# Kernel optimization log

Hardware: AMD Instinct MI355X
Metric: run time of the kernel (lower is better)

Reference implementation:

```python
import jax, jax.numpy as jnp
import numpy as np

N = 100000
E = 1600000
D_IN = 128
HEADS = 8
HEAD_DIM = 16  # hidden_channels // heads = 128 // 8
D_HID = HEADS * HEAD_DIM  # 128
D_OUT = 128
NEG_SLOPE = 0.2


def setup_inputs() -> dict:
    key = jax.random.key(0)
    ks = jax.random.split(key, 10)
    x = jax.random.normal(ks[0], (N, D_IN), dtype=jnp.float32)
    edge_index = jax.random.randint(ks[1], (2, E), 0, N, dtype=jnp.int64)
    s = 1.0 / np.sqrt(D_IN)
    W_gat = jax.random.uniform(ks[2], (D_IN, D_HID), minval=-s, maxval=s, dtype=jnp.float32)
    att_src = jax.random.uniform(ks[3], (HEADS, HEAD_DIM), minval=-s, maxval=s, dtype=jnp.float32)
    att_dst = jax.random.uniform(ks[4], (HEADS, HEAD_DIM), minval=-s, maxval=s, dtype=jnp.float32)
    b_gat = jnp.zeros((D_HID,), dtype=jnp.float32)
    so = 1.0 / np.sqrt(D_OUT)
    W_fc1 = jax.random.uniform(ks[5], (D_OUT, D_OUT), minval=-so, maxval=so, dtype=jnp.float32)
    b_fc1 = jax.random.uniform(ks[6], (D_OUT,), minval=-so, maxval=so, dtype=jnp.float32)
    W_fc2 = jax.random.uniform(ks[7], (D_OUT, D_OUT), minval=-so, maxval=so, dtype=jnp.float32)
    b_fc2 = jax.random.uniform(ks[8], (D_OUT,), minval=-so, maxval=so, dtype=jnp.float32)
    return {"x": x, "edge_index": edge_index, "W_gat": W_gat, "att_src": att_src,
            "att_dst": att_dst, "b_gat": b_gat, "W_fc1": W_fc1, "b_fc1": b_fc1,
            "W_fc2": W_fc2, "b_fc2": b_fc2}


def _gat_conv(x, src, dst, W_gat, att_src, att_dst, b_gat):
    n = x.shape[0]
    xp = (x @ W_gat).reshape(n, HEADS, HEAD_DIM)        # [N,H,C]
    a_src = jnp.einsum('nhc,hc->nh', xp, att_src)       # [N,H]
    a_dst = jnp.einsum('nhc,hc->nh', xp, att_dst)       # [N,H]
    e = jax.nn.leaky_relu(a_src[src] + a_dst[dst], NEG_SLOPE)  # [E,H]
    # segment softmax over edges grouped by destination node
    e_max = jax.ops.segment_max(e, dst, num_segments=n)
    e = jnp.exp(e - e_max[dst])
    e_sum = jax.ops.segment_sum(e, dst, num_segments=n)
    alpha = e / (e_sum[dst] + 1e-16)                    # [E,H]
    msg = xp[src] * alpha[:, :, None]                   # [E,H,C]
    out = jax.ops.segment_sum(msg, dst, num_segments=n) # [N,H,C]
    return out.reshape(n, D_HID) + b_gat


def reference(x, edge_index, W_gat, att_src, att_dst, b_gat, W_fc1, b_fc1, W_fc2, b_fc2):
    n = x.shape[0]
    # PyG GATConv default add_self_loops=True
    loops = jnp.arange(n, dtype=edge_index.dtype)
    src = jnp.concatenate([edge_index[0], loops])
    dst = jnp.concatenate([edge_index[1], loops])
    z = _gat_conv(x, src, dst, W_gat, att_src, att_dst, b_gat)
    z1 = z @ W_fc1 + b_fc1
    z2 = z @ W_fc2 + b_fc2
    return (z, z1, z2)
```

## Files before the change

kernel.cpp:

```cpp
#include <hip/hip_runtime.h>
#include <hip/hip_bf16.h>


#define NBUCK  256
#define BSHIFT 9
#define BNODES 512
#define IPB    8192

typedef __attribute__((ext_vector_type(8))) short bf16x8;
typedef __attribute__((ext_vector_type(4))) float f32x4;

static __device__ __forceinline__ short f2bf(float f) {
    __hip_bfloat16 h = __float2bfloat16(f);
    return *reinterpret_cast<short*>(&h);
}

__global__ __launch_bounds__(256) void k0_swizzle(
    const float* __restrict__ W0, const float* __restrict__ W1,
    const float* __restrict__ W2, const float* __restrict__ att_s,
    const float* __restrict__ att_d, unsigned short* __restrict__ S0,
    unsigned short* __restrict__ S1, unsigned short* __restrict__ S2,
    unsigned short* __restrict__ Sa, int* __restrict__ col_total)
{
    const int t = blockIdx.x * 256 + threadIdx.x;
    if (t < NBUCK) col_total[t] = 0;
    if (t < 3 * 2048) {
        const int m = t >> 11;
        const int r = t & 2047;
        const int tile = r >> 6;
        const int l    = r & 63;
        const int ks   = tile & 3;
        const int cb   = tile >> 2;
        const int c    = cb * 16 + (l & 15);
        const int kb   = ks * 32 + (l >> 4) * 8;
        const float* W = (m == 0) ? W0 : (m == 1) ? W1 : W2;
        unsigned short* S = (m == 0) ? S0 : (m == 1) ? S1 : S2;
        unsigned short* dst = S + ((size_t)tile * 64 + l) * 8;
#pragma unroll
        for (int j = 0; j < 8; ++j)
            dst[j] = (unsigned short)f2bf(W[(kb + j) * 128 + c]);
    } else if (t < 3 * 2048 + 256) {
        const int r  = t - 3 * 2048;
        const int ks = r >> 6;
        const int l  = r & 63;
        const int hp = l & 15;
        const int h  = hp & 7;
        const float* av = (hp < 8) ? (att_s + h * 16) : (att_d + h * 16);
        unsigned short* dst = Sa + ((size_t)ks * 64 + l) * 8;
#pragma unroll
        for (int j = 0; j < 8; ++j) {
            const int k = ks * 32 + (l >> 4) * 8 + j;
            float acc = 0.f;
#pragma unroll
            for (int u = 0; u < 16; ++u)
                acc += W0[k * 128 + h * 16 + u] * av[u];
            dst[j] = (unsigned short)f2bf(acc);
        }
    }
}

__global__ __launch_bounds__(256) void g1p1(
    const float* __restrict__ x, const unsigned short* __restrict__ Wswz,
    const unsigned short* __restrict__ Sa, unsigned short* __restrict__ xpb,
    float* __restrict__ a_src, float* __restrict__ a_dst,
    const int* __restrict__ ei, int* __restrict__ M, int* __restrict__ col_total,
    int n, int E, int g1b, int nblk)
{
    if ((int)blockIdx.x < g1b) {
        const int wid  = __builtin_amdgcn_readfirstlane(threadIdx.x >> 6);
        const int lane = threadIdx.x & 63;
        const int lr   = lane & 15;
        const int kg   = lane >> 4;
        const int rowbase = blockIdx.x * 128 + wid * 32;

        bf16x8 afr[2][4];
#pragma unroll
        for (int rt = 0; rt < 2; ++rt) {
            int row = rowbase + rt * 16 + lr;
            row = (row < n) ? row : (n - 1);
            const float* rp = x + (size_t)row * 128 + kg * 8;
#pragma unroll
            for (int ks = 0; ks < 4; ++ks) {
                const float4 v0 = *reinterpret_cast<const float4*>(rp + ks * 32);
                const float4 v1 = *reinterpret_cast<const float4*>(rp + ks * 32 + 4);
                bf16x8 a;
                a[0] = f2bf(v0.x); a[1] = f2bf(v0.y); a[2] = f2bf(v0.z); a[3] = f2bf(v0.w);
                a[4] = f2bf(v1.x); a[5] = f2bf(v1.y); a[6] = f2bf(v1.z); a[7] = f2bf(v1.w);
                afr[rt][ks] = a;
            }
        }

        f32x4 acc[2][8] = {};
#pragma unroll
        for (int cb = 0; cb < 8; ++cb) {
            const unsigned short* bp = Wswz + ((size_t)(cb * 4) * 64 + lane) * 8;
            bf16x8 bfr[4];
#pragma unroll
            for (int ks = 0; ks < 4; ++ks)
                bfr[ks] = *reinterpret_cast<const bf16x8*>(bp + (size_t)ks * 512);
#pragma unroll
            for (int ks = 0; ks < 4; ++ks) {
                acc[0][cb] = __builtin_amdgcn_mfma_f32_16x16x32_bf16(afr[0][ks], bfr[ks], acc[0][cb], 0, 0, 0);
                acc[1][cb] = __builtin_amdgcn_mfma_f32_16x16x32_bf16(afr[1][ks], bfr[ks], acc[1][cb], 0, 0, 0);
            }
        }

        f32x4 accs[2] = {};
#pragma unroll
        for (int ks = 0; ks < 4; ++ks) {
            const bf16x8 bs = *reinterpret_cast<const bf16x8*>(Sa + ((size_t)ks * 64 + lane) * 8);
            accs[0] = __builtin_amdgcn_mfma_f32_16x16x32_bf16(afr[0][ks], bs, accs[0], 0, 0, 0);
            accs[1] = __builtin_amdgcn_mfma_f32_16x16x32_bf16(afr[1][ks], bs, accs[1], 0, 0, 0);
        }

#pragma unroll
        for (int rt = 0; rt < 2; ++rt) {
#pragma unroll
            for (int reg = 0; reg < 4; ++reg) {
                const int row = rowbase + rt * 16 + kg * 4 + reg;
                if (row < n) {
                    unsigned short* op = xpb + (size_t)row * 128 + lr;
#pragma unroll
                    for (int cb = 0; cb < 8; ++cb)
                        op[cb * 16] = (unsigned short)f2bf(acc[rt][cb][reg]);
                    if (lr < 8) a_src[row * 8 + lr] = accs[rt][reg];
                    else        a_dst[row * 8 + (lr - 8)] = accs[rt][reg];
                }
            }
        }
    } else {
        __shared__ int h[NBUCK];
        const int pb  = blockIdx.x - g1b;
        const int tid = threadIdx.x;
        for (int k = tid; k < NBUCK; k += 256) h[k] = 0;
        __syncthreads();

        const int tot = E + n;
        const int base = pb * IPB;
        const int lim = (base + IPB < tot) ? base + IPB : tot;
        for (int j = base + tid; j < lim; j += 256) {
            const int d = (j < E) ? ei[E + j] : (j - E);
            atomicAdd(&h[d >> BSHIFT], 1);
        }
        __syncthreads();
        for (int k = tid; k < NBUCK; k += 256) {
            M[(size_t)k * nblk + pb] = h[k];
            if (h[k]) atomicAdd(&col_total[k], h[k]);
        }
    }
}

__global__ __launch_bounds__(256) void p2a_colscan(
    int* __restrict__ M, const int* __restrict__ col_total,
    int* __restrict__ bucket_ptr, int* __restrict__ row_ptr, int nblk, int N)
{
    const int b    = blockIdx.x;
    const int tid  = threadIdx.x;
    const int lane = tid & 63;
    const int wid  = tid >> 6;
    __shared__ int wsum[4];
    __shared__ int sbase;

    const int v0 = col_total[tid];
    int ws0 = v0;
#pragma unroll
    for (int off = 1; off < 64; off <<= 1) {
        const int t = __shfl_up(ws0, off);
        if (lane >= off) ws0 += t;
    }
    if (lane == 63) wsum[wid] = ws0;
    __syncthreads();
    int woff0 = 0;
    for (int w2 = 0; w2 < wid; ++w2) woff0 += wsum[w2];
    const int excl0 = woff0 + ws0 - v0;
    if (tid == b) sbase = excl0;
    if (b == NBUCK - 1 && tid == NBUCK - 1) {
        bucket_ptr[NBUCK] = excl0 + v0;
        row_ptr[N] = excl0 + v0;
    }
    __syncthreads();
    const int base = sbase;
    if (tid == 0) bucket_ptr[b] = base;
    __syncthreads();

    int carry = base;
    for (int bb = 0; bb < nblk; bb += 256) {
        const int idx = bb + tid;
        const int v = (idx < nblk) ? M[(size_t)b * nblk + idx] : 0;
        int ws = v;
#pragma unroll
        for (int off = 1; off < 64; off <<= 1) {
            const int t = __shfl_up(ws, off);
            if (lane >= off) ws += t;
        }
        if (lane == 63) wsum[wid] = ws;
        __syncthreads();
        int woff = 0;
        for (int w2 = 0; w2 < wid; ++w2) woff += wsum[w2];
        const int alltot = wsum[0] + wsum[1] + wsum[2] + wsum[3];
        if (idx < nblk) M[(size_t)b * nblk + idx] = carry + woff + ws - v;
        carry += alltot;
        __syncthreads();
    }
}

__global__ __launch_bounds__(256) void p3_scatter(
    const int* __restrict__ ei, const int* __restrict__ M,
    int* __restrict__ pairs, int E, int N, int nblk)
{
    __shared__ int lcnt[NBUCK];
    const int tid = threadIdx.x;
    for (int k = tid; k < NBUCK; k += 256) lcnt[k] = 0;
    __syncthreads();

    const int tot = E + N;
    const int base = blockIdx.x * IPB;
    const int lim = (base + IPB < tot) ? base + IPB : tot;
    for (int j = base + tid; j < lim; j += 256) {
        int s, d;
        if (j < E) { s = ei[j]; d = ei[E + j]; }
        else       { s = j - E; d = s; }
        const int b = d >> BSHIFT;
        const int r = atomicAdd(&lcnt[b], 1);
        const int pos = M[(size_t)b * nblk + blockIdx.x] + r;
        pairs[pos] = s | ((d & (BNODES - 1)) << 17);
    }
}

__global__ __launch_bounds__(256) void p4_finalize(
    const int* __restrict__ pairs, const int* __restrict__ bucket_ptr,
    int* __restrict__ row_ptr, int* __restrict__ csr_src, int N)
{
    const int b     = blockIdx.x;
    const int node0 = b << BSHIFT;
    const int beg   = bucket_ptr[b];
    const int end   = bucket_ptr[b + 1];
    const int tid   = threadIdx.x;
    const int lane  = tid & 63;
    const int wid   = tid >> 6;

    __shared__ int hist[BNODES];
    __shared__ int exc[BNODES];
    __shared__ int cnt2[BNODES];
    __shared__ int wsum[4];

    for (int k = tid; k < BNODES; k += 256) { hist[k] = 0; cnt2[k] = 0; }
    __syncthreads();

    for (int i = beg + tid; i < end; i += 256)
        atomicAdd(&hist[pairs[i] >> 17], 1);
    __syncthreads();

    const int a0 = hist[2 * tid];
    const int a1 = hist[2 * tid + 1];
    const int s  = a0 + a1;
    int ws = s;
#pragma unroll
    for (int off = 1; off < 64; off <<= 1) {
        const int t = __shfl_up(ws, off);
        if (lane >= off) ws += t;
    }
    if (lane == 63) wsum[wid] = ws;
    __syncthreads();
    int woff = 0;
    for (int w2 = 0; w2 < wid; ++w2) woff += wsum[w2];
    const int e0 = woff + ws - s;
    exc[2 * tid]     = e0;
    exc[2 * tid + 1] = e0 + a0;
    __syncthreads();

    for (int k = tid; k < BNODES; k += 256) {
        const int node = node0 + k;
        if (node < N) row_ptr[node] = beg + exc[k];
    }
    for (int i = beg + tid; i < end; i += 256) {
        const int v  = pairs[i];
        const int dl = v >> 17;
        const int r  = atomicAdd(&cnt2[dl], 1);
        csr_src[beg + exc[dl] + r] = v & 0x1FFFF;
    }
}

__global__ __launch_bounds__(256) void k5_aggregate(
    const unsigned short* __restrict__ xpb, const float* __restrict__ a_src,
    const float* __restrict__ a_dst, const int* __restrict__ row_ptr,
    const int* __restrict__ csr_src, const float* __restrict__ b_gat,
    float* __restrict__ z, unsigned int* __restrict__ zb, int n)
{
    const int wave = blockIdx.x * 4 + __builtin_amdgcn_readfirstlane(threadIdx.x >> 6);
    if (wave >= n) return;
    const int lane = threadIdx.x & 63;
    const int d = wave;
    const int beg = row_ptr[d];
    const int end = row_ptr[d + 1];
    const int h = lane >> 3;
    const float adst = a_dst[d * 8 + h];
    const int co = 2 * lane;

    float l0 = 0.f, l1 = 0.f;
    float ax0 = 0.f, ay0 = 0.f, ax1 = 0.f, ay1 = 0.f;

    for (int i = beg; i < end; i += 8) {
        int ss[8];
        unsigned int xv[8];
        float pv[8];
#pragma unroll
        for (int j = 0; j < 8; ++j) {
            const int idx = i + j;
            ss[j] = csr_src[(idx < end) ? idx : (end - 1)];
        }
#pragma unroll
        for (int j = 0; j < 8; ++j)
            xv[j] = *reinterpret_cast<const unsigned int*>(xpb + (size_t)ss[j] * 128 + co);
#pragma unroll
        for (int j = 0; j < 8; ++j) {
            float v = a_src[ss[j] * 8 + h] + adst;
            v = (v > 0.f) ? v : 0.2f * v;
            const float e = __expf(v);
            pv[j] = (i + j < end) ? e : 0.f;
        }
#pragma unroll
        for (int j = 0; j < 8; ++j) {
            const float cx = __uint_as_float(xv[j] << 16);
            const float cy = __uint_as_float(xv[j] & 0xffff0000u);
            if (j & 1) {
                l1 += pv[j];
                ax1 = fmaf(pv[j], cx, ax1);
                ay1 = fmaf(pv[j], cy, ay1);
            } else {
                l0 += pv[j];
                ax0 = fmaf(pv[j], cx, ax0);
                ay0 = fmaf(pv[j], cy, ay0);
            }
        }
    }

    const float inv = 1.0f / (l0 + l1 + 1e-16f);
    const float2 bg = *reinterpret_cast<const float2*>(&b_gat[co]);
    float2 o;
    o.x = (ax0 + ax1) * inv + bg.x;
    o.y = (ay0 + ay1) * inv + bg.y;
    *reinterpret_cast<float2*>(&z[(size_t)d * 128 + co]) = o;
    const unsigned int pk = ((unsigned int)(unsigned short)f2bf(o.y) << 16) |
                            (unsigned int)(unsigned short)f2bf(o.x);
    zb[(size_t)d * 64 + lane] = pk;
}

__global__ __launch_bounds__(256) void g2_mfma_fc(
    const unsigned int* __restrict__ zb,
    const unsigned short* __restrict__ S1, const unsigned short* __restrict__ S2,
    const float* __restrict__ b1, const float* __restrict__ b2,
    float* __restrict__ z1, float* __restrict__ z2, int n)
{
    const int wid  = __builtin_amdgcn_readfirstlane(threadIdx.x >> 6);
    const int lane = threadIdx.x & 63;
    const int lr   = lane & 15;
    const int kg   = lane >> 4;
    const int rowbase = blockIdx.x * 128 + wid * 32;

    bf16x8 afr[2][4];
#pragma unroll
    for (int rt = 0; rt < 2; ++rt) {
        int row = rowbase + rt * 16 + lr;
        row = (row < n) ? row : (n - 1);
        const unsigned short* rp = (const unsigned short*)(zb + (size_t)row * 64) + kg * 8;
#pragma unroll
        for (int ks = 0; ks < 4; ++ks)
            afr[rt][ks] = *reinterpret_cast<const bf16x8*>(rp + ks * 32);
    }

    f32x4 acc1[2][8] = {};
    f32x4 acc2[2][8] = {};
#pragma unroll
    for (int cb = 0; cb < 8; ++cb) {
        const unsigned short* bp1 = S1 + ((size_t)(cb * 4) * 64 + lane) * 8;
        const unsigned short* bp2 = S2 + ((size_t)(cb * 4) * 64 + lane) * 8;
        bf16x8 f1[4], f2v[4];
#pragma unroll
        for (int ks = 0; ks < 4; ++ks) {
            f1[ks]  = *reinterpret_cast<const bf16x8*>(bp1 + (size_t)ks * 512);
            f2v[ks] = *reinterpret_cast<const bf16x8*>(bp2 + (size_t)ks * 512);
        }
#pragma unroll
        for (int ks = 0; ks < 4; ++ks) {
            acc1[0][cb] = __builtin_amdgcn_mfma_f32_16x16x32_bf16(afr[0][ks], f1[ks],  acc1[0][cb], 0, 0, 0);
            acc1[1][cb] = __builtin_amdgcn_mfma_f32_16x16x32_bf16(afr[1][ks], f1[ks],  acc1[1][cb], 0, 0, 0);
            acc2[0][cb] = __builtin_amdgcn_mfma_f32_16x16x32_bf16(afr[0][ks], f2v[ks], acc2[0][cb], 0, 0, 0);
            acc2[1][cb] = __builtin_amdgcn_mfma_f32_16x16x32_bf16(afr[1][ks], f2v[ks], acc2[1][cb], 0, 0, 0);
        }
    }

    float bb1[8], bb2[8];
#pragma unroll
    for (int cb = 0; cb < 8; ++cb) { bb1[cb] = b1[cb * 16 + lr]; bb2[cb] = b2[cb * 16 + lr]; }

#pragma unroll
    for (int rt = 0; rt < 2; ++rt) {
#pragma unroll
        for (int reg = 0; reg < 4; ++reg) {
            const int row = rowbase + rt * 16 + kg * 4 + reg;
            if (row < n) {
                float* o1 = z1 + (size_t)row * 128 + lr;
                float* o2 = z2 + (size_t)row * 128 + lr;
#pragma unroll
                for (int cb = 0; cb < 8; ++cb) {
                    o1[cb * 16] = acc1[rt][cb][reg] + bb1[cb];
                    o2[cb * 16] = acc2[rt][cb][reg] + bb2[cb];
                }
            }
        }
    }
}

extern "C" void kernel_launch(void* const* d_in, const int* in_sizes, int n_in,
                              void* d_out, int out_size, void* d_ws, size_t ws_size,
                              hipStream_t stream)
{
    const float* x       = (const float*)d_in[0];
    const int*   ei      = (const int*)  d_in[1];
    const float* W_gat   = (const float*)d_in[2];
    const float* att_src = (const float*)d_in[3];
    const float* att_dst = (const float*)d_in[4];
    const float* b_gat   = (const float*)d_in[5];
    const float* W_fc1   = (const float*)d_in[6];
    const float* b_fc1   = (const float*)d_in[7];
    const float* W_fc2   = (const float*)d_in[8];
    const float* b_fc2   = (const float*)d_in[9];

    const int N = in_sizes[0] / 128;
    const int E = in_sizes[1] / 2;
    const int tot = E + N;
    const int nblk = (tot + IPB - 1) / IPB;
    const int nbuck_used = (N + BNODES - 1) >> BSHIFT;
    const int g1b = (N + 127) / 128;

    char* w = (char*)d_ws;
    unsigned short* xpb = (unsigned short*)w;  w += (size_t)N * 128 * 2;
    unsigned int* zb = (unsigned int*)w;       w += (size_t)N * 64 * 4;
    float* a_src  = (float*)w;  w += (size_t)N * 8 * 4;
    float* a_dst  = (float*)w;  w += (size_t)N * 8 * 4;
    int* row_ptr  = (int*)w;    w += (size_t)(N + 1) * 4;
    w = (char*)(((size_t)w + 15) & ~(size_t)15);
    unsigned short* S0 = (unsigned short*)w; w += 16384 * 2;
    unsigned short* S1 = (unsigned short*)w; w += 16384 * 2;
    unsigned short* S2 = (unsigned short*)w; w += 16384 * 2;
    unsigned short* Sa = (unsigned short*)w; w += 2048 * 2;
    int* M          = (int*)w;  w += (size_t)nblk * NBUCK * 4;
    int* col_total  = (int*)w;  w += NBUCK * 4;
    int* bucket_ptr = (int*)w;  w += (NBUCK + 1) * 4;
    w = (char*)(((size_t)w + 15) & ~(size_t)15);
    int* pairs    = (int*)w;    w += (size_t)tot * 4;
    int* csr_src  = (int*)w;    w += (size_t)tot * 4;

    float* z  = (float*)d_out;
    float* z1 = z  + (size_t)N * 128;
    float* z2 = z1 + (size_t)N * 128;

    k0_swizzle<<<(3 * 2048 + 256 + 255) / 256, 256, 0, stream>>>(
        W_gat, W_fc1, W_fc2, att_src, att_dst, S0, S1, S2, Sa, col_total);

    g1p1<<<g1b + nblk, 256, 0, stream>>>(x, S0, Sa, xpb, a_src, a_dst,
                                         ei, M, col_total, N, E, g1b, nblk);

    p2a_colscan<<<NBUCK, 256, 0, stream>>>(M, col_total, bucket_ptr, row_ptr, nblk, N);
    p3_scatter<<<nblk, 256, 0, stream>>>(ei, M, pairs, E, N, nblk);
    p4_finalize<<<nbuck_used, 256, 0, stream>>>(pairs, bucket_ptr, row_ptr, csr_src, N);

    k5_aggregate<<<(N + 3) / 4, 256, 0, stream>>>(xpb, a_src, a_dst, row_ptr, csr_src,
                                                  b_gat, z, zb, N);

    g2_mfma_fc<<<(N + 127) / 128, 256, 0, stream>>>(zb, S1, S2, b_fc1, b_fc2, z1, z2, N);
}
```

Baseline: 204.8 us.

## Precompute per-edge bf16 attention exponentials in CSR finalize, stream them in aggregate

The CSR finalize kernel now computes, for every edge and all 8 heads, the leaky-relu and exp of a_src+a_dst. It stores the results as bf16 in a per-edge array laid out in CSR order. The aggregate kernel then reads these weights sequentially instead of gathering a_src per source and recomputing exp, and uses readfirstlane to make row bounds and source indices scalar. This trades a random gather plus exp in the hot loop for an extra 16 bytes per edge written and read, adds a random a_src gather in the finalize kernel, and lowers the precision of the attention weights to bf16.

```diff
diff --git a/kernel.cpp b/kernel.cpp
--- a/kernel.cpp
+++ b/kernel.cpp
@@ -229,7 +229,9 @@
 
 __global__ __launch_bounds__(256) void p4_finalize(
     const int* __restrict__ pairs, const int* __restrict__ bucket_ptr,
-    int* __restrict__ row_ptr, int* __restrict__ csr_src, int N)
+    const float* __restrict__ a_src, const float* __restrict__ a_dst,
+    int* __restrict__ row_ptr, int* __restrict__ csr_src,
+    unsigned short* __restrict__ e_exp, int N)
 {
     const int b     = blockIdx.x;
     const int node0 = b << BSHIFT;
@@ -276,25 +278,50 @@
     for (int i = beg + tid; i < end; i += 256) {
         const int v  = pairs[i];
         const int dl = v >> 17;
+        const int sv = v & 0x1FFFF;
         const int r  = atomicAdd(&cnt2[dl], 1);
-        csr_src[beg + exc[dl] + r] = v & 0x1FFFF;
+        const int pos = beg + exc[dl] + r;
+        csr_src[pos] = sv;
+
+        const float4 as0 = *reinterpret_cast<const float4*>(a_src + (size_t)sv * 8);
+        const float4 as1 = *reinterpret_cast<const float4*>(a_src + (size_t)sv * 8 + 4);
+        const float4 ad0 = *reinterpret_cast<const float4*>(a_dst + (size_t)(node0 + dl) * 8);
+        const float4 ad1 = *reinterpret_cast<const float4*>(a_dst + (size_t)(node0 + dl) * 8 + 4);
+        float vv[8];
+        vv[0] = as0.x + ad0.x; vv[1] = as0.y + ad0.y;
+        vv[2] = as0.z + ad0.z; vv[3] = as0.w + ad0.w;
+        vv[4] = as1.x + ad1.x; vv[5] = as1.y + ad1.y;
+        vv[6] = as1.z + ad1.z; vv[7] = as1.w + ad1.w;
+        unsigned int pk[4];
+#pragma unroll
+        for (int q = 0; q < 4; ++q) {
+            float u0 = vv[2 * q],     e0f;
+            float u1 = vv[2 * q + 1], e1f;
+            u0 = (u0 > 0.f) ? u0 : 0.2f * u0;
+            u1 = (u1 > 0.f) ? u1 : 0.2f * u1;
+            e0f = __expf(u0);
+            e1f = __expf(u1);
+            pk[q] = ((unsigned int)(unsigned short)f2bf(e1f) << 16) |
+                    (unsigned int)(unsigned short)f2bf(e0f);
+        }
+        *reinterpret_cast<int4*>(e_exp + (size_t)pos * 8) =
+            make_int4((int)pk[0], (int)pk[1], (int)pk[2], (int)pk[3]);
     }
 }
 
 __global__ __launch_bounds__(256) void k5_aggregate(
-    const unsigned short* __restrict__ xpb, const float* __restrict__ a_src,
-    const float* __restrict__ a_dst, const int* __restrict__ row_ptr,
-    const int* __restrict__ csr_src, const float* __restrict__ b_gat,
-    float* __restrict__ z, unsigned int* __restrict__ zb, int n)
+    const unsigned short* __restrict__ xpb, const unsigned short* __restrict__ e_exp,
+    const int* __restrict__ row_ptr, const int* __restrict__ csr_src,
+    const float* __restrict__ b_gat, float* __restrict__ z,
+    unsigned int* __restrict__ zb, int n)
 {
     const int wave = blockIdx.x * 4 + __builtin_amdgcn_readfirstlane(threadIdx.x >> 6);
     if (wave >= n) return;
     const int lane = threadIdx.x & 63;
     const int d = wave;
-    const int beg = row_ptr[d];
-    const int end = row_ptr[d + 1];
+    const int beg = __builtin_amdgcn_readfirstlane(row_ptr[d]);
+    const int end = __builtin_amdgcn_readfirstlane(row_ptr[d + 1]);
     const int h = lane >> 3;
-    const float adst = a_dst[d * 8 + h];
     const int co = 2 * lane;
 
     float l0 = 0.f, l1 = 0.f;
@@ -302,35 +329,31 @@
 
     for (int i = beg; i < end; i += 8) {
         int ss[8];
+        float pw[8];
         unsigned int xv[8];
-        float pv[8];
 #pragma unroll
         for (int j = 0; j < 8; ++j) {
-            const int idx = i + j;
-            ss[j] = csr_src[(idx < end) ? idx : (end - 1)];
+            const int idx = (i + j < end) ? (i + j) : (end - 1);
+            ss[j] = __builtin_amdgcn_readfirstlane(csr_src[idx]);
+            const unsigned int pu = (unsigned int)e_exp[(size_t)idx * 8 + h] << 16;
+            const float p = __uint_as_float(pu);
+            pw[j] = (i + j < end) ? p : 0.f;
         }
 #pragma unroll
         for (int j = 0; j < 8; ++j)
             xv[j] = *reinterpret_cast<const unsigned int*>(xpb + (size_t)ss[j] * 128 + co);
-#pragma unroll
-        for (int j = 0; j < 8; ++j) {
-            float v = a_src[ss[j] * 8 + h] + adst;
-            v = (v > 0.f) ? v : 0.2f * v;
-            const float e = __expf(v);
-            pv[j] = (i + j < end) ? e : 0.f;
-        }
 #pragma unroll
         for (int j = 0; j < 8; ++j) {
             const float cx = __uint_as_float(xv[j] << 16);
             const float cy = __uint_as_float(xv[j] & 0xffff0000u);
             if (j & 1) {
-                l1 += pv[j];
-                ax1 = fmaf(pv[j], cx, ax1);
-                ay1 = fmaf(pv[j], cy, ay1);
+                l1 += pw[j];
+                ax1 = fmaf(pw[j], cx, ax1);
+                ay1 = fmaf(pw[j], cy, ay1);
             } else {
-                l0 += pv[j];
-                ax0 = fmaf(pv[j], cx, ax0);
-                ay0 = fmaf(pv[j], cy, ay0);
+                l0 += pw[j];
+                ax0 = fmaf(pw[j], cx, ax0);
+                ay0 = fmaf(pw[j], cy, ay0);
             }
         }
     }
@@ -451,6 +474,8 @@
     w = (char*)(((size_t)w + 15) & ~(size_t)15);
     int* pairs    = (int*)w;    w += (size_t)tot * 4;
     int* csr_src  = (int*)w;    w += (size_t)tot * 4;
+    w = (char*)(((size_t)w + 15) & ~(size_t)15);
+    unsigned short* e_exp = (unsigned short*)w; w += (size_t)tot * 8 * 2;
 
     float* z  = (float*)d_out;
     float* z1 = z  + (size_t)N * 128;
@@ -464,9 +489,10 @@
 
     p2a_colscan<<<NBUCK, 256, 0, stream>>>(M, col_total, bucket_ptr, row_ptr, nblk, N);
     p3_scatter<<<nblk, 256, 0, stream>>>(ei, M, pairs, E, N, nblk);
-    p4_finalize<<<nbuck_used, 256, 0, stream>>>(pairs, bucket_ptr, row_ptr, csr_src, N);
-
-    k5_aggregate<<<(N + 3) / 4, 256, 0, stream>>>(xpb, a_src, a_dst, row_ptr, csr_src,
+    p4_finalize<<<nbuck_used, 256, 0, stream>>>(pairs, bucket_ptr, a_src, a_dst,
+                                                row_ptr, csr_src, e_exp, N);
+
+    k5_aggregate<<<(N + 3) / 4, 256, 0, stream>>>(xpb, e_exp, row_ptr, csr_src,
                                                   b_gat, z, zb, N);
 
     g2_mfma_fc<<<(N + 127) / 128, 256, 0, stream>>>(zb, S1, S2, b_fc1, b_fc2, z1, z2, N);
```

Measured after the change: 236.0 us. 1.15x slower.
